# Kernel optimization log

Measured on AMD Instinct MI355X. Metric: run time of the kernel, lower is better.

## Reference

```python
import jax, jax.numpy as jnp
import numpy as np

BIG = 1e6
EPS = 1e-12


def _normalize(x):
    return x / (jnp.linalg.norm(x, axis=-1, keepdims=True) + EPS)


def _euclidean_dist(x, y):
    # x: [m, d], y: [n, d] -> [m, n]
    xx = jnp.sum(x * x, axis=1, keepdims=True)          # [m, 1]
    yy = jnp.sum(y * y, axis=1)[None, :]                # [1, n]
    d = xx + yy - 2.0 * (x @ y.T)
    return jnp.sqrt(jnp.clip(d, EPS, None))


def _cam_loss(embeddings, labels, centers_value, centers_cnt, margin):
    B, D = embeddings.shape
    C = centers_value.shape[0]

    # --- _Cup: centroid scatter-reduce update (detached in original) ---
    emb_d = jax.lax.stop_gradient(embeddings)
    sums = jax.ops.segment_sum(emb_d, labels, num_segments=C)              # [C, D]
    counts = jax.ops.segment_sum(jnp.ones((B,), emb_d.dtype), labels,
                                 num_segments=C)                           # [C]
    upd_val = jax.lax.stop_gradient(centers_value) + sums
    upd_cnt = jax.lax.stop_gradient(centers_cnt) + counts[:, None]
    centers = jnp.where(upd_cnt > 0, upd_val / jnp.maximum(upd_cnt, 1.0), 0.0)

    centers = _normalize(centers)
    emb = _normalize(embeddings)

    pd = _euclidean_dist(emb, emb)        # [B, B]
    pdc = _euclidean_dist(emb, centers)   # [B, C]

    # masks
    eye = jnp.eye(B, dtype=bool)
    labels_eq = labels[None, :] == labels[:, None]
    mask_ap = (~eye) & labels_eq          # anchor-positive [B, B]
    mask_an = ~labels_eq                  # anchor-negative [B, B]
    classes = jnp.arange(C)
    mask_ap_c = labels[:, None] == classes[None, :]   # [B, C]
    mask_an_c = ~mask_ap_c

    # hardest positive
    hp = jnp.max(mask_ap * pd, axis=1, keepdims=True)
    hp_c = jnp.max(mask_ap_c * pdc, axis=1, keepdims=True)
    hpos = jnp.maximum(hp, hp_c)                       # [B, 1]
    hpos_d = jax.lax.stop_gradient(hpos)

    # hardest negative: outside the positive boundary
    greater = pd > hpos_d
    greater_c = pdc > hpos_d
    gbm = mask_an & greater
    gbm_c = mask_an_c & greater_c
    neg_out = jnp.min(pd + BIG * (~gbm), axis=1, keepdims=True)
    neg_out_c = jnp.min(pdc + BIG * (~gbm_c), axis=1, keepdims=True)
    h_out = jnp.minimum(neg_out, neg_out_c)

    # hardest negative: inside (rows with no negative beyond the boundary)
    ms = jnp.sum(gbm, axis=1) == 0        # [B]
    ms_c = jnp.sum(gbm_c, axis=1) == 0
    neg_in = jnp.max(jnp.where(ms[:, None], pd, BIG) * mask_an,
                     axis=1, keepdims=True)
    neg_in_c = jnp.max(jnp.where(ms_c[:, None], pdc, BIG) * mask_an_c,
                       axis=1, keepdims=True)
    h_in = jnp.maximum(neg_in, neg_in_c)

    hneg = jnp.minimum(h_out, h_in)       # [B, 1]

    # MarginRankingLoss(dist_an, dist_ap, y=1, reduction='sum') / B
    loss = jnp.sum(jax.nn.relu(hpos - hneg + margin)) / B
    return loss


def setup_inputs() -> dict:
    key = jax.random.key(0)
    k1, k2 = jax.random.split(key)
    B, D, C = 4096, 2048, 1024
    return {
        "embeddings": jax.random.normal(k1, (B, D), dtype=jnp.float32),
        "labels": jax.random.randint(k2, (B,), 0, C),
        "centers_value": jnp.zeros((C, D), dtype=jnp.float32),
        "centers_cnt": jnp.zeros((C, D), dtype=jnp.float32),
        "margin": jnp.float32(1.0),
    }


def reference(embeddings, labels, centers_value, centers_cnt, margin):
    return _cam_loss(embeddings, labels, centers_value, centers_cnt, margin)
```

## Files before the change

### kernel.cpp

```cpp
#include <hip/hip_runtime.h>
#include <hip/hip_bf16.h>


typedef __attribute__((ext_vector_type(8))) short short8;
typedef __attribute__((ext_vector_type(4))) float f32x4;

#define BIGF 1e6f
#define EPSC 1e-12f

__device__ __forceinline__ float bf2f(unsigned short u){
  unsigned int x = ((unsigned int)u) << 16;
  return __uint_as_float(x);
}
__device__ __forceinline__ unsigned short f2bf(float f){
  __hip_bfloat16 h = __float2bfloat16(f);
  return *reinterpret_cast<unsigned short*>(&h);
}

#define GLL16(gptr, lptr) \
  __builtin_amdgcn_global_load_lds( \
      (const __attribute__((address_space(1))) unsigned int*)(gptr), \
      (__attribute__((address_space(3))) unsigned int*)(lptr), 16, 0, 0)

#define VMWAIT(S) asm volatile("s_waitcnt " S ::: "memory")
#define SBAR()    asm volatile("s_barrier" ::: "memory")

__global__ __launch_bounds__(256) void k_setup(const int* __restrict__ labels,
    int* cnt, int* members,
    unsigned* mn0, unsigned* mx0, unsigned* fl0,
    unsigned* mn1, unsigned* mx1, unsigned* fl1,
    int B, int C, int MMAX){
  int gid = blockIdx.x * blockDim.x + threadIdx.x;
  unsigned bigbits = __float_as_uint(BIGF);
  if (gid < B){
    mn0[gid] = bigbits; mx0[gid] = 0u; fl0[gid] = 0u;
    mn1[gid] = bigbits; mx1[gid] = 0u; fl1[gid] = 0u;
  }
  int w = threadIdx.x >> 6, lane = threadIdx.x & 63;
  int c = blockIdx.x * 4 + w;
  if (c >= C) return;
  int base = 0;
  int nit = (B + 63) >> 6;
  for (int itc = 0; itc < nit; ++itc){
    int idx = itc * 64 + lane;
    int lab = (idx < B) ? labels[idx] : -1;
    unsigned long long m = __ballot(lab == c);
    if (lab == c){
      int rk = base + (int)__popcll(m & ((1ull << lane) - 1ull));
      if (rk < MMAX) members[c * MMAX + rk] = idx;
    }
    base += (int)__popcll(m);
  }
  if (lane == 0) cnt[c] = base;
}

template<int R>
__global__ __launch_bounds__(256) void k_prep(const float* __restrict__ emb,
    const float* __restrict__ cval, const float* __restrict__ ccnt,
    const int* __restrict__ cnt, const int* __restrict__ members,
    unsigned short* __restrict__ enb, unsigned short* __restrict__ cnb,
    float* __restrict__ exx, float* __restrict__ cxx,
    int D, int MMAX, int nbNorm){
  int w = threadIdx.x >> 6, lane = threadIdx.x & 63;
  if ((int)blockIdx.x < nbNorm){
    int i = blockIdx.x * 4 + w;
    const float* row = emb + (size_t)i * D;
    float v[R][8];
    float ss = 0.f;
    #pragma unroll
    for (int r = 0; r < R; ++r){
      int base = r * 512 + lane * 8;
      float4 a = *reinterpret_cast<const float4*>(&row[base]);
      float4 b = *reinterpret_cast<const float4*>(&row[base + 4]);
      v[r][0]=a.x; v[r][1]=a.y; v[r][2]=a.z; v[r][3]=a.w;
      v[r][4]=b.x; v[r][5]=b.y; v[r][6]=b.z; v[r][7]=b.w;
      #pragma unroll
      for (int k = 0; k < 8; ++k) ss += v[r][k] * v[r][k];
    }
    #pragma unroll
    for (int s = 1; s < 64; s <<= 1) ss += __shfl_xor(ss, s);
    float inv = 1.f / (sqrtf(ss) + EPSC);
    unsigned short* orow = enb + (size_t)i * D;
    int xr = (i & 7) << 3;
    #pragma unroll
    for (int r = 0; r < R; ++r){
      int base = (r * 512 + lane * 8) ^ xr;
      short8 o;
      #pragma unroll
      for (int k = 0; k < 8; ++k) o[k] = (short)f2bf(v[r][k] * inv);
      *reinterpret_cast<short8*>(&orow[base]) = o;
    }
    if (lane == 0) exx[i] = ss * inv * inv;
  } else {
    int c = ((int)blockIdx.x - nbNorm) * 4 + w;
    int n = cnt[c], m = n < MMAX ? n : MMAX;
    float acc[R][8];
    #pragma unroll
    for (int r = 0; r < R; ++r)
      #pragma unroll
      for (int k = 0; k < 8; ++k) acc[r][k] = 0.f;
    for (int e = 0; e < m; ++e){
      const float* row = emb + (size_t)members[c * MMAX + e] * D;
      #pragma unroll
      for (int r = 0; r < R; ++r){
        int base = r * 512 + lane * 8;
        float4 a = *reinterpret_cast<const float4*>(&row[base]);
        float4 b = *reinterpret_cast<const float4*>(&row[base + 4]);
        acc[r][0]+=a.x; acc[r][1]+=a.y; acc[r][2]+=a.z; acc[r][3]+=a.w;
        acc[r][4]+=b.x; acc[r][5]+=b.y; acc[r][6]+=b.z; acc[r][7]+=b.w;
      }
    }
    float cf = (float)n;
    float ss = 0.f;
    #pragma unroll
    for (int r = 0; r < R; ++r){
      int base = r * 512 + lane * 8;
      float4 u0 = *reinterpret_cast<const float4*>(&ccnt[(size_t)c * D + base]);
      float4 u1 = *reinterpret_cast<const float4*>(&ccnt[(size_t)c * D + base + 4]);
      float4 w0 = *reinterpret_cast<const float4*>(&cval[(size_t)c * D + base]);
      float4 w1 = *reinterpret_cast<const float4*>(&cval[(size_t)c * D + base + 4]);
      float uc[8] = {u0.x,u0.y,u0.z,u0.w,u1.x,u1.y,u1.z,u1.w};
      float wv[8] = {w0.x,w0.y,w0.z,w0.w,w1.x,w1.y,w1.z,w1.w};
      #pragma unroll
      for (int k = 0; k < 8; ++k){
        float u = uc[k] + cf;
        float vv = wv[k] + acc[r][k];
        float ce = (u > 0.f) ? (vv / fmaxf(u, 1.f)) : 0.f;
        acc[r][k] = ce; ss += ce * ce;
      }
    }
    #pragma unroll
    for (int s = 1; s < 64; s <<= 1) ss += __shfl_xor(ss, s);
    float inv = 1.f / (sqrtf(ss) + EPSC);
    int xr = (c & 7) << 3;
    #pragma unroll
    for (int r = 0; r < R; ++r){
      int base = (r * 512 + lane * 8) ^ xr;
      short8 o;
      #pragma unroll
      for (int k = 0; k < 8; ++k) o[k] = (short)f2bf(acc[r][k] * inv);
      *reinterpret_cast<short8*>(&cnb[(size_t)c * D + base]) = o;
    }
    if (lane == 0) cxx[c] = ss * inv * inv;
  }
}

template<int NCH>
__global__ __launch_bounds__(256) void k_hpos(const unsigned short* __restrict__ enb,
    const unsigned short* __restrict__ cnb, const float* __restrict__ exx,
    const float* __restrict__ cxx, const int* __restrict__ labels,
    const int* __restrict__ cnt, const int* __restrict__ members,
    float* __restrict__ hpos, int D, int MMAX){
  int w = threadIdx.x >> 6, lane = threadIdx.x & 63;
  int i = blockIdx.x * 4 + w;
  int li = labels[i];
  const unsigned short* arow = enb + (size_t)i * D;
  int xri = (i & 7) << 3;
  float av[NCH][8];
  #pragma unroll
  for (int ch = 0; ch < NCH; ++ch){
    short8 a8 = *reinterpret_cast<const short8*>(&arow[(ch * 512 + lane * 8) ^ xri]);
    #pragma unroll
    for (int k = 0; k < 8; ++k) av[ch][k] = bf2f((unsigned short)a8[k]);
  }
  float xi = exx[i];
  float hp = 0.f;
  int m = cnt[li] < MMAX ? cnt[li] : MMAX;
  for (int e = 0; e < m; ++e){
    int j = members[li * MMAX + e];
    if (j == i) continue;
    const unsigned short* brow = enb + (size_t)j * D;
    int xrj = (j & 7) << 3;
    float p = 0.f;
    #pragma unroll
    for (int ch = 0; ch < NCH; ++ch){
      short8 b8 = *reinterpret_cast<const short8*>(&brow[(ch * 512 + lane * 8) ^ xrj]);
      #pragma unroll
      for (int k = 0; k < 8; ++k) p += av[ch][k] * bf2f((unsigned short)b8[k]);
    }
    #pragma unroll
    for (int s = 1; s < 64; s <<= 1) p += __shfl_xor(p, s);
    float d2 = xi + exx[j] - 2.f * p;
    hp = fmaxf(hp, sqrtf(fmaxf(d2, EPSC)));
  }
  {
    const unsigned short* brow = cnb + (size_t)li * D;
    int xrc = (li & 7) << 3;
    float p = 0.f;
    #pragma unroll
    for (int ch = 0; ch < NCH; ++ch){
      short8 b8 = *reinterpret_cast<const short8*>(&brow[(ch * 512 + lane * 8) ^ xrc]);
      #pragma unroll
      for (int k = 0; k < 8; ++k) p += av[ch][k] * bf2f((unsigned short)b8[k]);
    }
    #pragma unroll
    for (int s = 1; s < 64; s <<= 1) p += __shfl_xor(p, s);
    float d2 = xi + cxx[li] - 2.f * p;
    hp = fmaxf(hp, sqrtf(fmaxf(d2, EPSC)));
  }
  if (lane == 0) hpos[i] = hp;
}

#define PD_STAGE(SB, KIND, KT) do { \
    unsigned short* dst_ = (SB) + (KIND) * 8192 + wid * (16 * 64); \
    const unsigned short* src_ = ((KIND) < 2 \
        ? gA + (size_t)((KIND) * 128) * D \
        : gB + (size_t)(((KIND) - 2) * 128) * D) + (KT); \
    GLL16(src_, dst_); \
    GLL16(src_ + (size_t)8 * D, dst_ + 8 * 64); \
  } while (0)

#define RD_A(DST, HP) do { \
    _Pragma("unroll") \
    for (int m_ = 0; m_ < 4; ++m_){ \
      DST[m_][0] = *reinterpret_cast<const short8*>(&(HP)[aoff[m_][0]]); \
      DST[m_][1] = *reinterpret_cast<const short8*>(&(HP)[aoff[m_][1]]); \
    } } while (0)

#define RD_B(HP) do { \
    _Pragma("unroll") \
    for (int n_ = 0; n_ < 2; ++n_){ \
      b[n_][0] = *reinterpret_cast<const short8*>(&(HP)[boff[n_][0]]); \
      b[n_][1] = *reinterpret_cast<const short8*>(&(HP)[boff[n_][1]]); \
    } } while (0)

#define LGKM0() do { VMWAIT("lgkmcnt(0)"); __builtin_amdgcn_sched_barrier(0); } while (0)

#define MFMA16(AV, MH, NH) do { \
    __builtin_amdgcn_s_setprio(1); \
    _Pragma("unroll") \
    for (int m_ = 0; m_ < 4; ++m_) \
      _Pragma("unroll") \
      for (int n_ = 0; n_ < 2; ++n_) \
        _Pragma("unroll") \
        for (int ks_ = 0; ks_ < 2; ++ks_) \
          acc[MH][NH][m_][n_] = __builtin_amdgcn_mfma_f32_16x16x32_bf16( \
              AV[m_][ks_], b[n_][ks_], acc[MH][NH][m_][n_], 0, 0, 0); \
    __builtin_amdgcn_s_setprio(0); } while (0)

__global__ __launch_bounds__(512, 2) void k_pd_all(
    const unsigned short* __restrict__ enb,
    const unsigned short* __restrict__ cnb,
    const float* __restrict__ exx, const float* __restrict__ cxx,
    const int* __restrict__ labels, const float* __restrict__ hpos,
    unsigned* __restrict__ mn0, unsigned* __restrict__ mx0, unsigned* __restrict__ fl0,
    unsigned* __restrict__ mn1, unsigned* __restrict__ mx1, unsigned* __restrict__ fl1,
    int D, int nTri, int nby, int nCx)
{
  extern __shared__ unsigned short sm[];
  const int nwg = gridDim.x;
  const int orig = blockIdx.x;
  const int q8 = nwg >> 3, r8 = nwg & 7;
  const int xcd = orig & 7, idx = orig >> 3;
  const int t = (xcd < r8 ? xcd * (q8 + 1) : r8 * (q8 + 1) + (xcd - r8) * q8) + idx;

  const bool pdc = (t >= nTri);
  int bx, by;
  if (!pdc){
    if ((nby & 3) == 0){
      int gb = 0, cb = 0, rem = t;
      for (;;){
        int sz = (cb < gb) ? 16 : 10;
        if (rem < sz) break;
        rem -= sz;
        if (++cb > gb){ cb = 0; ++gb; }
      }
      if (cb < gb){
        by = gb * 4 + (rem >> 2);
        bx = cb * 4 + (rem & 3);
      } else {
        int r = 0;
        while (((r + 1) * (r + 2)) / 2 <= rem) ++r;
        by = gb * 4 + r;
        bx = cb * 4 + (rem - (r * (r + 1)) / 2);
      }
    } else {
      int b_ = (int)((sqrtf(8.f * (float)t + 1.f) - 1.f) * 0.5f);
      while ((b_ + 1) * (b_ + 2) / 2 <= t) ++b_;
      while (b_ * (b_ + 1) / 2 > t) --b_;
      by = b_; bx = t - b_ * (b_ + 1) / 2;
    }
  } else {
    int u = t - nTri;
    by = u / nCx; bx = u - by * nCx;
  }
  const unsigned short* cmat = pdc ? cnb : enb;
  const float* cxv = pdc ? cxx : exx;
  unsigned* mnv = pdc ? mn1 : mn0;
  unsigned* mxv = pdc ? mx1 : mx0;
  unsigned* flv = pdc ? fl1 : fl0;

  const int j0 = bx * 256, i0 = by * 256;
  const int tid = threadIdx.x;
  const int wid = tid >> 6, lane = tid & 63;
  const int wr = wid >> 2, wc = wid & 3;
  const int lr = lane & 15, lg = lane >> 4;

  const int srow = wid * 16 + (lane >> 3);
  const int scol = (lane & 7) * 8;
  const unsigned short* gA = enb  + (size_t)(i0 + srow) * D + scol;
  const unsigned short* gB = cmat + (size_t)(j0 + srow) * D + scol;

  int aoff[4][2], boff[2][2];
  #pragma unroll
  for (int m = 0; m < 4; ++m){
    int ra = wr * 64 + m * 16 + lr;
    #pragma unroll
    for (int ks = 0; ks < 2; ++ks)
      aoff[m][ks] = ra * 64 + ((ks * 32 + lg * 8) ^ ((ra & 7) << 3));
  }
  #pragma unroll
  for (int n = 0; n < 2; ++n){
    int rb = wc * 32 + n * 16 + lr;
    #pragma unroll
    for (int ks = 0; ks < 2; ++ks)
      boff[n][ks] = rb * 64 + ((ks * 32 + lg * 8) ^ ((rb & 7) << 3));
  }

  f32x4 acc[2][2][4][2];
  #pragma unroll
  for (int mh = 0; mh < 2; ++mh)
    #pragma unroll
    for (int nh = 0; nh < 2; ++nh)
      #pragma unroll
      for (int m = 0; m < 4; ++m)
        #pragma unroll
        for (int n = 0; n < 2; ++n)
          acc[mh][nh][m][n] = (f32x4){0.f, 0.f, 0.f, 0.f};

  short8 a0[4][2], a1[4][2], b[2][2];

  const int nt = D >> 6;
  PD_STAGE(sm, 0, 0); PD_STAGE(sm, 1, 0); PD_STAGE(sm, 2, 0); PD_STAGE(sm, 3, 0);
  VMWAIT("vmcnt(0)");
  SBAR();

  for (int it = 0; it < nt; ++it){
    const unsigned short* db = sm + (size_t)(it & 1) * 32768;
    unsigned short* sb = sm + (size_t)((it & 1) ^ 1) * 32768;
    const bool hn = (it + 1 < nt);
    const int ktn = (it + 1) << 6;
    RD_A(a0, db);
    RD_B(db + 2 * 8192);
    if (hn){ PD_STAGE(sb, 0, ktn); VMWAIT("vmcnt(4)"); } else { VMWAIT("vmcnt(4)"); }
    SBAR();
    LGKM0();
    MFMA16(a0, 0, 0);
    RD_A(a1, db + 8192);
    if (hn){ PD_STAGE(sb, 2, ktn); VMWAIT("vmcnt(4)"); } else { VMWAIT("vmcnt(2)"); }
    SBAR();
    LGKM0();
    MFMA16(a1, 1, 0);
    RD_B(db + 3 * 8192);
    if (hn){ PD_STAGE(sb, 1, ktn); VMWAIT("vmcnt(4)"); } else { VMWAIT("vmcnt(0)"); }
    SBAR();
    LGKM0();
    MFMA16(a1, 1, 1);
    if (hn){ PD_STAGE(sb, 3, ktn); VMWAIT("vmcnt(4)"); }
    SBAR();
    MFMA16(a0, 0, 1);
  }

  const bool docol = (!pdc) && (bx != by);
  int jl[2][2]; float xj[2][2], hpj[2][2];
  #pragma unroll
  for (int nh = 0; nh < 2; ++nh)
    #pragma unroll
    for (int n = 0; n < 2; ++n){
      int j = j0 + nh * 128 + wc * 32 + n * 16 + lr;
      jl[nh][n] = pdc ? j : labels[j];
      xj[nh][n] = cxv[j];
      hpj[nh][n] = docol ? hpos[j] : 0.f;
    }
  float cmn[2][2], cmx[2][2]; int cfl[2][2];
  #pragma unroll
  for (int nh = 0; nh < 2; ++nh)
    #pragma unroll
    for (int n = 0; n < 2; ++n){ cmn[nh][n] = BIGF; cmx[nh][n] = 0.f; cfl[nh][n] = 0; }

  #pragma unroll
  for (int mh = 0; mh < 2; ++mh)
    #pragma unroll
    for (int m = 0; m < 4; ++m)
      #pragma unroll
      for (int r = 0; r < 4; ++r){
        int i = i0 + mh * 128 + wr * 64 + m * 16 + lg * 4 + r;
        int li = labels[i];
        float xi = exx[i];
        float hpi = hpos[i];
        float mn = BIGF, mx = 0.f; int fl = 0;
        #pragma unroll
        for (int nh = 0; nh < 2; ++nh)
          #pragma unroll
          for (int n = 0; n < 2; ++n){
            float d2 = xi + xj[nh][n] - 2.f * acc[mh][nh][m][n][r];
            float d  = sqrtf(fmaxf(d2, EPSC));
            bool an = (li != jl[nh][n]);
            bool g  = an && (d > hpi);
            mn = fminf(mn, g ? d : BIGF);
            mx = fmaxf(mx, an ? d : 0.f);
            fl |= (g ? 1 : 0) | (an ? 2 : 0);
            if (docol){
              bool gc = an && (d > hpj[nh][n]);
              cmn[nh][n] = fminf(cmn[nh][n], gc ? d : BIGF);
              cmx[nh][n] = fmaxf(cmx[nh][n], an ? d : 0.f);
              cfl[nh][n] |= (gc ? 1 : 0) | (an ? 2 : 0);
            }
          }
        #pragma unroll
        for (int s = 1; s < 16; s <<= 1){
          mn = fminf(mn, __shfl_xor(mn, s));
          mx = fmaxf(mx, __shfl_xor(mx, s));
          fl |= __shfl_xor(fl, s);
        }
        if (lr == 0){
          atomicMin(&mnv[i], __float_as_uint(mn));
          atomicMax(&mxv[i], __float_as_uint(mx));
          if (fl) atomicOr(&flv[i], (unsigned)fl);
        }
      }
  if (docol){
    #pragma unroll
    for (int nh = 0; nh < 2; ++nh)
      #pragma unroll
      for (int n = 0; n < 2; ++n){
        float mn = cmn[nh][n], mx = cmx[nh][n]; int fl = cfl[nh][n];
        #pragma unroll
        for (int s = 16; s < 64; s <<= 1){
          mn = fminf(mn, __shfl_xor(mn, s));
          mx = fmaxf(mx, __shfl_xor(mx, s));
          fl |= __shfl_xor(fl, s);
        }
        if (lg == 0){
          int j = j0 + nh * 128 + wc * 32 + n * 16 + lr;
          atomicMin(&mn0[j], __float_as_uint(mn));
          atomicMax(&mx0[j], __float_as_uint(mx));
          if (fl) atomicOr(&fl0[j], (unsigned)fl);
        }
      }
  }
}

__global__ __launch_bounds__(1024) void k_final(const float* __restrict__ hpos,
    const unsigned* __restrict__ mn0, const unsigned* __restrict__ mx0,
    const unsigned* __restrict__ fl0, const unsigned* __restrict__ mn1,
    const unsigned* __restrict__ mx1, const unsigned* __restrict__ fl1,
    const float* __restrict__ margin, float* __restrict__ out, int B){
  __shared__ float red[16];
  float part = 0.f;
  float mar = margin[0];
  for (int i = threadIdx.x; i < B; i += blockDim.x){
    float h_out = fminf(__uint_as_float(mn0[i]), __uint_as_float(mn1[i]));
    unsigned f0 = fl0[i], f1 = fl1[i];
    float ni  = (!(f0 & 1u)) ? __uint_as_float(mx0[i]) : ((f0 & 2u) ? BIGF : 0.f);
    float nic = (!(f1 & 1u)) ? __uint_as_float(mx1[i]) : ((f1 & 2u) ? BIGF : 0.f);
    float h_in = fmaxf(ni, nic);
    float hneg = fminf(h_out, h_in);
    float t = hpos[i] - hneg + mar;
    part += fmaxf(t, 0.f);
  }
  #pragma unroll
  for (int s = 32; s; s >>= 1) part += __shfl_xor(part, s);
  if ((threadIdx.x & 63) == 0) red[threadIdx.x >> 6] = part;
  __syncthreads();
  if (threadIdx.x == 0){
    float tot = 0.f;
    int nw = blockDim.x >> 6;
    for (int k = 0; k < nw; ++k) tot += red[k];
    out[0] = tot / (float)B;
  }
}

extern "C" void kernel_launch(void* const* d_in, const int* in_sizes, int n_in,
                              void* d_out, int out_size, void* d_ws, size_t ws_size,
                              hipStream_t stream){
  const float* emb    = (const float*)d_in[0];
  const int*   labels = (const int*)d_in[1];
  const float* cval   = (const float*)d_in[2];
  const float* ccnt   = (const float*)d_in[3];
  const float* margin = (const float*)d_in[4];
  float* out = (float*)d_out;

  int B = in_sizes[1];
  int D = in_sizes[0] / B;
  int C = in_sizes[2] / D;
  const int MMAX = 64;

  char* ws = (char*)d_ws;
  size_t off = 0;
  auto alloc = [&](size_t bytes)->char*{
    char* p = ws + off;
    off = (off + bytes + 255) & ~(size_t)255;
    return p;
  };
  unsigned short* enb = (unsigned short*)alloc((size_t)B * D * 2);
  unsigned short* cnb = (unsigned short*)alloc((size_t)C * D * 2);
  float* exx  = (float*)alloc((size_t)B * 4);
  float* cxx  = (float*)alloc((size_t)C * 4);
  float* hpos = (float*)alloc((size_t)B * 4);
  unsigned* mn0 = (unsigned*)alloc((size_t)B * 4);
  unsigned* mx0 = (unsigned*)alloc((size_t)B * 4);
  unsigned* fl0 = (unsigned*)alloc((size_t)B * 4);
  unsigned* mn1 = (unsigned*)alloc((size_t)B * 4);
  unsigned* mx1 = (unsigned*)alloc((size_t)B * 4);
  unsigned* fl1 = (unsigned*)alloc((size_t)B * 4);
  int* cnt     = (int*)alloc((size_t)C * 4);
  int* members = (int*)alloc((size_t)C * MMAX * 4);
  (void)ws_size; (void)n_in; (void)out_size;

  hipFuncSetAttribute((const void*)k_pd_all,
                      hipFuncAttributeMaxDynamicSharedMemorySize, 131072);

  int nbSetup = (C + 3) / 4;
  int nbInit  = ((B > C ? B : C) + 255) / 256;
  if (nbInit > nbSetup) nbSetup = nbInit;
  k_setup<<<nbSetup, 256, 0, stream>>>(labels, cnt, members,
                                       mn0, mx0, fl0, mn1, mx1, fl1, B, C, MMAX);

  int nbNorm = B / 4, nbCent = C / 4;
  int R = D >> 9;
  if (R == 4){
    k_prep<4><<<nbNorm + nbCent, 256, 0, stream>>>(emb, cval, ccnt, cnt, members,
                                                   enb, cnb, exx, cxx, D, MMAX, nbNorm);
  } else if (R == 2){
    k_prep<2><<<nbNorm + nbCent, 256, 0, stream>>>(emb, cval, ccnt, cnt, members,
                                                   enb, cnb, exx, cxx, D, MMAX, nbNorm);
  } else {
    k_prep<1><<<nbNorm + nbCent, 256, 0, stream>>>(emb, cval, ccnt, cnt, members,
                                                   enb, cnb, exx, cxx, D, MMAX, nbNorm);
  }

  switch (R){
    case 1: k_hpos<1><<<B/4, 256, 0, stream>>>(enb, cnb, exx, cxx, labels, cnt, members, hpos, D, MMAX); break;
    case 2: k_hpos<2><<<B/4, 256, 0, stream>>>(enb, cnb, exx, cxx, labels, cnt, members, hpos, D, MMAX); break;
    default: k_hpos<4><<<B/4, 256, 0, stream>>>(enb, cnb, exx, cxx, labels, cnt, members, hpos, D, MMAX); break;
  }

  int nby = B / 256, nCx = C / 256;
  int nTri = nby * (nby + 1) / 2;
  k_pd_all<<<nTri + nby * nCx, 512, 131072, stream>>>(
      enb, cnb, exx, cxx, labels, hpos,
      mn0, mx0, fl0, mn1, mx1, fl1, D, nTri, nby, nCx);
  k_final<<<1, 1024, 0, stream>>>(hpos, mn0, mx0, fl0, mn1, mx1, fl1, margin, out, B);
}
```

Measured before the change: 145.8 us.

## Fuse class membership, centroid and hardest-positive into one per-class kernel

Replaces the setup, prep and per-row hardest-positive kernels with a normalize kernel and a per-class kernel. The per-class kernel builds the member list in shared memory, computes the centroid, then evaluates each member pair once (symmetric) plus the member-centroid distance, keeping the centroid in LDS. This removes one launch, the global members and count arrays, and the duplicated pair dot products. In exchange the per-class work is serialized within one wave, with only C/4 blocks, so parallelism may be lower.

```diff
diff --git a/kernel.cpp b/kernel.cpp
--- a/kernel.cpp
+++ b/kernel.cpp
@@ -25,180 +25,168 @@
 #define VMWAIT(S) asm volatile("s_waitcnt " S ::: "memory")
 #define SBAR()    asm volatile("s_barrier" ::: "memory")
 
-__global__ __launch_bounds__(256) void k_setup(const int* __restrict__ labels,
-    int* cnt, int* members,
-    unsigned* mn0, unsigned* mx0, unsigned* fl0,
-    unsigned* mn1, unsigned* mx1, unsigned* fl1,
-    int B, int C, int MMAX){
-  int gid = blockIdx.x * blockDim.x + threadIdx.x;
-  unsigned bigbits = __float_as_uint(BIGF);
-  if (gid < B){
-    mn0[gid] = bigbits; mx0[gid] = 0u; fl0[gid] = 0u;
-    mn1[gid] = bigbits; mx1[gid] = 0u; fl1[gid] = 0u;
-  }
+template<int R>
+__global__ __launch_bounds__(256) void k_norm(const float* __restrict__ emb,
+    unsigned short* __restrict__ enb, float* __restrict__ exx,
+    unsigned* __restrict__ mn0, unsigned* __restrict__ mx0, unsigned* __restrict__ fl0,
+    unsigned* __restrict__ mn1, unsigned* __restrict__ mx1, unsigned* __restrict__ fl1,
+    int D){
   int w = threadIdx.x >> 6, lane = threadIdx.x & 63;
-  int c = blockIdx.x * 4 + w;
+  int i = blockIdx.x * 4 + w;
+  if (lane == 0){
+    unsigned bigbits = __float_as_uint(BIGF);
+    mn0[i] = bigbits; mx0[i] = 0u; fl0[i] = 0u;
+    mn1[i] = bigbits; mx1[i] = 0u; fl1[i] = 0u;
+  }
+  const float* row = emb + (size_t)i * D;
+  float v[R][8];
+  float ss = 0.f;
+  #pragma unroll
+  for (int r = 0; r < R; ++r){
+    int base = r * 512 + lane * 8;
+    float4 a = *reinterpret_cast<const float4*>(&row[base]);
+    float4 b = *reinterpret_cast<const float4*>(&row[base + 4]);
+    v[r][0]=a.x; v[r][1]=a.y; v[r][2]=a.z; v[r][3]=a.w;
+    v[r][4]=b.x; v[r][5]=b.y; v[r][6]=b.z; v[r][7]=b.w;
+    #pragma unroll
+    for (int k = 0; k < 8; ++k) ss += v[r][k] * v[r][k];
+  }
+  #pragma unroll
+  for (int s = 1; s < 64; s <<= 1) ss += __shfl_xor(ss, s);
+  float inv = 1.f / (sqrtf(ss) + EPSC);
+  unsigned short* orow = enb + (size_t)i * D;
+  int xr = (i & 7) << 3;
+  #pragma unroll
+  for (int r = 0; r < R; ++r){
+    int base = (r * 512 + lane * 8) ^ xr;
+    short8 o;
+    #pragma unroll
+    for (int k = 0; k < 8; ++k) o[k] = (short)f2bf(v[r][k] * inv);
+    *reinterpret_cast<short8*>(&orow[base]) = o;
+  }
+  if (lane == 0) exx[i] = ss * inv * inv;
+}
+
+template<int R>
+__global__ __launch_bounds__(256) void k_cls(const float* __restrict__ emb,
+    const float* __restrict__ cval, const float* __restrict__ ccnt,
+    const int* __restrict__ labels, const unsigned short* __restrict__ enb,
+    const float* __restrict__ exx,
+    unsigned short* __restrict__ cnb, float* __restrict__ cxx,
+    float* __restrict__ hpos, int B, int D, int C){
+  __shared__ int memL[4][64];
+  __shared__ float hpL[4][64];
+  __shared__ unsigned short cenL[4][R * 512];
+  int wid = threadIdx.x >> 6, lane = threadIdx.x & 63;
+  int c = blockIdx.x * 4 + wid;
   if (c >= C) return;
-  int base = 0;
+  int n = 0;
   int nit = (B + 63) >> 6;
   for (int itc = 0; itc < nit; ++itc){
     int idx = itc * 64 + lane;
     int lab = (idx < B) ? labels[idx] : -1;
-    unsigned long long m = __ballot(lab == c);
+    unsigned long long bm = __ballot(lab == c);
     if (lab == c){
-      int rk = base + (int)__popcll(m & ((1ull << lane) - 1ull));
-      if (rk < MMAX) members[c * MMAX + rk] = idx;
-    }
-    base += (int)__popcll(m);
-  }
-  if (lane == 0) cnt[c] = base;
-}
-
-template<int R>
-__global__ __launch_bounds__(256) void k_prep(const float* __restrict__ emb,
-    const float* __restrict__ cval, const float* __restrict__ ccnt,
-    const int* __restrict__ cnt, const int* __restrict__ members,
-    unsigned short* __restrict__ enb, unsigned short* __restrict__ cnb,
-    float* __restrict__ exx, float* __restrict__ cxx,
-    int D, int MMAX, int nbNorm){
-  int w = threadIdx.x >> 6, lane = threadIdx.x & 63;
-  if ((int)blockIdx.x < nbNorm){
-    int i = blockIdx.x * 4 + w;
-    const float* row = emb + (size_t)i * D;
-    float v[R][8];
-    float ss = 0.f;
+      int rk = n + (int)__popcll(bm & ((1ull << lane) - 1ull));
+      if (rk < 64) memL[wid][rk] = idx;
+    }
+    n += (int)__popcll(bm);
+  }
+  int m = n < 64 ? n : 64;
+  hpL[wid][lane] = 0.f;
+  float acc[R][8];
+  #pragma unroll
+  for (int r = 0; r < R; ++r)
+    #pragma unroll
+    for (int k = 0; k < 8; ++k) acc[r][k] = 0.f;
+  for (int e = 0; e < m; ++e){
+    const float* row = emb + (size_t)memL[wid][e] * D;
     #pragma unroll
     for (int r = 0; r < R; ++r){
       int base = r * 512 + lane * 8;
       float4 a = *reinterpret_cast<const float4*>(&row[base]);
       float4 b = *reinterpret_cast<const float4*>(&row[base + 4]);
-      v[r][0]=a.x; v[r][1]=a.y; v[r][2]=a.z; v[r][3]=a.w;
-      v[r][4]=b.x; v[r][5]=b.y; v[r][6]=b.z; v[r][7]=b.w;
+      acc[r][0]+=a.x; acc[r][1]+=a.y; acc[r][2]+=a.z; acc[r][3]+=a.w;
+      acc[r][4]+=b.x; acc[r][5]+=b.y; acc[r][6]+=b.z; acc[r][7]+=b.w;
+    }
+  }
+  float cf = (float)n;
+  float ss = 0.f;
+  #pragma unroll
+  for (int r = 0; r < R; ++r){
+    int base = r * 512 + lane * 8;
+    float4 u0 = *reinterpret_cast<const float4*>(&ccnt[(size_t)c * D + base]);
+    float4 u1 = *reinterpret_cast<const float4*>(&ccnt[(size_t)c * D + base + 4]);
+    float4 w0 = *reinterpret_cast<const float4*>(&cval[(size_t)c * D + base]);
+    float4 w1 = *reinterpret_cast<const float4*>(&cval[(size_t)c * D + base + 4]);
+    float uc[8] = {u0.x,u0.y,u0.z,u0.w,u1.x,u1.y,u1.z,u1.w};
+    float wv[8] = {w0.x,w0.y,w0.z,w0.w,w1.x,w1.y,w1.z,w1.w};
+    #pragma unroll
+    for (int k = 0; k < 8; ++k){
+      float u = uc[k] + cf;
+      float vv = wv[k] + acc[r][k];
+      float ce = (u > 0.f) ? (vv / fmaxf(u, 1.f)) : 0.f;
+      acc[r][k] = ce; ss += ce * ce;
+    }
+  }
+  #pragma unroll
+  for (int s = 1; s < 64; s <<= 1) ss += __shfl_xor(ss, s);
+  float inv = 1.f / (sqrtf(ss) + EPSC);
+  float xc = ss * inv * inv;
+  int xr = (c & 7) << 3;
+  #pragma unroll
+  for (int r = 0; r < R; ++r){
+    int lin = r * 512 + lane * 8;
+    short8 o;
+    #pragma unroll
+    for (int k = 0; k < 8; ++k) o[k] = (short)f2bf(acc[r][k] * inv);
+    *reinterpret_cast<short8*>(&cnb[(size_t)c * D + (lin ^ xr)]) = o;
+    *reinterpret_cast<short8*>(&cenL[wid][lin]) = o;
+  }
+  if (lane == 0) cxx[c] = xc;
+  for (int e1 = 0; e1 < m; ++e1){
+    int i1 = memL[wid][e1];
+    int xr1 = (i1 & 7) << 3;
+    const unsigned short* row1 = enb + (size_t)i1 * D;
+    float av[R][8];
+    #pragma unroll
+    for (int r = 0; r < R; ++r){
+      short8 v = *reinterpret_cast<const short8*>(&row1[(r * 512 + lane * 8) ^ xr1]);
       #pragma unroll
-      for (int k = 0; k < 8; ++k) ss += v[r][k] * v[r][k];
-    }
-    #pragma unroll
-    for (int s = 1; s < 64; s <<= 1) ss += __shfl_xor(ss, s);
-    float inv = 1.f / (sqrtf(ss) + EPSC);
-    unsigned short* orow = enb + (size_t)i * D;
-    int xr = (i & 7) << 3;
-    #pragma unroll
-    for (int r = 0; r < R; ++r){
-      int base = (r * 512 + lane * 8) ^ xr;
-      short8 o;
+      for (int k = 0; k < 8; ++k) av[r][k] = bf2f((unsigned short)v[k]);
+    }
+    float x1 = exx[i1];
+    float hp = hpL[wid][e1];
+    for (int e2 = e1 + 1; e2 <= m; ++e2){
+      float p = 0.f, x2;
+      if (e2 < m){
+        int i2 = memL[wid][e2];
+        int xr2 = (i2 & 7) << 3;
+        const unsigned short* row2 = enb + (size_t)i2 * D;
+        #pragma unroll
+        for (int r = 0; r < R; ++r){
+          short8 v = *reinterpret_cast<const short8*>(&row2[(r * 512 + lane * 8) ^ xr2]);
+          #pragma unroll
+          for (int k = 0; k < 8; ++k) p += av[r][k] * bf2f((unsigned short)v[k]);
+        }
+        x2 = exx[i2];
+      } else {
+        #pragma unroll
+        for (int r = 0; r < R; ++r){
+          short8 v = *reinterpret_cast<const short8*>(&cenL[wid][r * 512 + lane * 8]);
+          #pragma unroll
+          for (int k = 0; k < 8; ++k) p += av[r][k] * bf2f((unsigned short)v[k]);
+        }
+        x2 = xc;
+      }
       #pragma unroll
-      for (int k = 0; k < 8; ++k) o[k] = (short)f2bf(v[r][k] * inv);
-      *reinterpret_cast<short8*>(&orow[base]) = o;
-    }
-    if (lane == 0) exx[i] = ss * inv * inv;
-  } else {
-    int c = ((int)blockIdx.x - nbNorm) * 4 + w;
-    int n = cnt[c], m = n < MMAX ? n : MMAX;
-    float acc[R][8];
-    #pragma unroll
-    for (int r = 0; r < R; ++r)
-      #pragma unroll
-      for (int k = 0; k < 8; ++k) acc[r][k] = 0.f;
-    for (int e = 0; e < m; ++e){
-      const float* row = emb + (size_t)members[c * MMAX + e] * D;
-      #pragma unroll
-      for (int r = 0; r < R; ++r){
-        int base = r * 512 + lane * 8;
-        float4 a = *reinterpret_cast<const float4*>(&row[base]);
-        float4 b = *reinterpret_cast<const float4*>(&row[base + 4]);
-        acc[r][0]+=a.x; acc[r][1]+=a.y; acc[r][2]+=a.z; acc[r][3]+=a.w;
-        acc[r][4]+=b.x; acc[r][5]+=b.y; acc[r][6]+=b.z; acc[r][7]+=b.w;
-      }
-    }
-    float cf = (float)n;
-    float ss = 0.f;
-    #pragma unroll
-    for (int r = 0; r < R; ++r){
-      int base = r * 512 + lane * 8;
-      float4 u0 = *reinterpret_cast<const float4*>(&ccnt[(size_t)c * D + base]);
-      float4 u1 = *reinterpret_cast<const float4*>(&ccnt[(size_t)c * D + base + 4]);
-      float4 w0 = *reinterpret_cast<const float4*>(&cval[(size_t)c * D + base]);
-      float4 w1 = *reinterpret_cast<const float4*>(&cval[(size_t)c * D + base + 4]);
-      float uc[8] = {u0.x,u0.y,u0.z,u0.w,u1.x,u1.y,u1.z,u1.w};
-      float wv[8] = {w0.x,w0.y,w0.z,w0.w,w1.x,w1.y,w1.z,w1.w};
-      #pragma unroll
-      for (int k = 0; k < 8; ++k){
-        float u = uc[k] + cf;
-        float vv = wv[k] + acc[r][k];
-        float ce = (u > 0.f) ? (vv / fmaxf(u, 1.f)) : 0.f;
-        acc[r][k] = ce; ss += ce * ce;
-      }
-    }
-    #pragma unroll
-    for (int s = 1; s < 64; s <<= 1) ss += __shfl_xor(ss, s);
-    float inv = 1.f / (sqrtf(ss) + EPSC);
-    int xr = (c & 7) << 3;
-    #pragma unroll
-    for (int r = 0; r < R; ++r){
-      int base = (r * 512 + lane * 8) ^ xr;
-      short8 o;
-      #pragma unroll
-      for (int k = 0; k < 8; ++k) o[k] = (short)f2bf(acc[r][k] * inv);
-      *reinterpret_cast<short8*>(&cnb[(size_t)c * D + base]) = o;
-    }
-    if (lane == 0) cxx[c] = ss * inv * inv;
-  }
-}
-
-template<int NCH>
-__global__ __launch_bounds__(256) void k_hpos(const unsigned short* __restrict__ enb,
-    const unsigned short* __restrict__ cnb, const float* __restrict__ exx,
-    const float* __restrict__ cxx, const int* __restrict__ labels,
-    const int* __restrict__ cnt, const int* __restrict__ members,
-    float* __restrict__ hpos, int D, int MMAX){
-  int w = threadIdx.x >> 6, lane = threadIdx.x & 63;
-  int i = blockIdx.x * 4 + w;
-  int li = labels[i];
-  const unsigned short* arow = enb + (size_t)i * D;
-  int xri = (i & 7) << 3;
-  float av[NCH][8];
-  #pragma unroll
-  for (int ch = 0; ch < NCH; ++ch){
-    short8 a8 = *reinterpret_cast<const short8*>(&arow[(ch * 512 + lane * 8) ^ xri]);
-    #pragma unroll
-    for (int k = 0; k < 8; ++k) av[ch][k] = bf2f((unsigned short)a8[k]);
-  }
-  float xi = exx[i];
-  float hp = 0.f;
-  int m = cnt[li] < MMAX ? cnt[li] : MMAX;
-  for (int e = 0; e < m; ++e){
-    int j = members[li * MMAX + e];
-    if (j == i) continue;
-    const unsigned short* brow = enb + (size_t)j * D;
-    int xrj = (j & 7) << 3;
-    float p = 0.f;
-    #pragma unroll
-    for (int ch = 0; ch < NCH; ++ch){
-      short8 b8 = *reinterpret_cast<const short8*>(&brow[(ch * 512 + lane * 8) ^ xrj]);
-      #pragma unroll
-      for (int k = 0; k < 8; ++k) p += av[ch][k] * bf2f((unsigned short)b8[k]);
-    }
-    #pragma unroll
-    for (int s = 1; s < 64; s <<= 1) p += __shfl_xor(p, s);
-    float d2 = xi + exx[j] - 2.f * p;
-    hp = fmaxf(hp, sqrtf(fmaxf(d2, EPSC)));
-  }
-  {
-    const unsigned short* brow = cnb + (size_t)li * D;
-    int xrc = (li & 7) << 3;
-    float p = 0.f;
-    #pragma unroll
-    for (int ch = 0; ch < NCH; ++ch){
-      short8 b8 = *reinterpret_cast<const short8*>(&brow[(ch * 512 + lane * 8) ^ xrc]);
-      #pragma unroll
-      for (int k = 0; k < 8; ++k) p += av[ch][k] * bf2f((unsigned short)b8[k]);
-    }
-    #pragma unroll
-    for (int s = 1; s < 64; s <<= 1) p += __shfl_xor(p, s);
-    float d2 = xi + cxx[li] - 2.f * p;
-    hp = fmaxf(hp, sqrtf(fmaxf(d2, EPSC)));
-  }
-  if (lane == 0) hpos[i] = hp;
+      for (int s = 1; s < 64; s <<= 1) p += __shfl_xor(p, s);
+      float d = sqrtf(fmaxf(x1 + x2 - 2.f * p, EPSC));
+      hp = fmaxf(hp, d);
+      if (e2 < m && lane == 0) hpL[wid][e2] = fmaxf(hpL[wid][e2], d);
+    }
+    if (lane == 0) hpos[i1] = hp;
+  }
 }
 
 #define PD_STAGE(SB, KIND, KT) do { \
@@ -484,7 +472,6 @@
   int B = in_sizes[1];
   int D = in_sizes[0] / B;
   int C = in_sizes[2] / D;
-  const int MMAX = 64;
 
   char* ws = (char*)d_ws;
   size_t off = 0;
@@ -504,36 +491,24 @@
   unsigned* mn1 = (unsigned*)alloc((size_t)B * 4);
   unsigned* mx1 = (unsigned*)alloc((size_t)B * 4);
   unsigned* fl1 = (unsigned*)alloc((size_t)B * 4);
-  int* cnt     = (int*)alloc((size_t)C * 4);
-  int* members = (int*)alloc((size_t)C * MMAX * 4);
   (void)ws_size; (void)n_in; (void)out_size;
 
   hipFuncSetAttribute((const void*)k_pd_all,
                       hipFuncAttributeMaxDynamicSharedMemorySize, 131072);
 
-  int nbSetup = (C + 3) / 4;
-  int nbInit  = ((B > C ? B : C) + 255) / 256;
-  if (nbInit > nbSetup) nbSetup = nbInit;
-  k_setup<<<nbSetup, 256, 0, stream>>>(labels, cnt, members,
-                                       mn0, mx0, fl0, mn1, mx1, fl1, B, C, MMAX);
-
-  int nbNorm = B / 4, nbCent = C / 4;
   int R = D >> 9;
   if (R == 4){
-    k_prep<4><<<nbNorm + nbCent, 256, 0, stream>>>(emb, cval, ccnt, cnt, members,
-                                                   enb, cnb, exx, cxx, D, MMAX, nbNorm);
+    k_norm<4><<<B/4, 256, 0, stream>>>(emb, enb, exx, mn0, mx0, fl0, mn1, mx1, fl1, D);
+    k_cls<4><<<(C + 3) / 4, 256, 0, stream>>>(emb, cval, ccnt, labels, enb, exx,
+                                              cnb, cxx, hpos, B, D, C);
   } else if (R == 2){
-    k_prep<2><<<nbNorm + nbCent, 256, 0, stream>>>(emb, cval, ccnt, cnt, members,
-                                                   enb, cnb, exx, cxx, D, MMAX, nbNorm);
+    k_norm<2><<<B/4, 256, 0, stream>>>(emb, enb, exx, mn0, mx0, fl0, mn1, mx1, fl1, D);
+    k_cls<2><<<(C + 3) / 4, 256, 0, stream>>>(emb, cval, ccnt, labels, enb, exx,
+                                              cnb, cxx, hpos, B, D, C);
   } else {
-    k_prep<1><<<nbNorm + nbCent, 256, 0, stream>>>(emb, cval, ccnt, cnt, members,
-                                                   enb, cnb, exx, cxx, D, MMAX, nbNorm);
-  }
-
-  switch (R){
-    case 1: k_hpos<1><<<B/4, 256, 0, stream>>>(enb, cnb, exx, cxx, labels, cnt, members, hpos, D, MMAX); break;
-    case 2: k_hpos<2><<<B/4, 256, 0, stream>>>(enb, cnb, exx, cxx, labels, cnt, members, hpos, D, MMAX); break;
-    default: k_hpos<4><<<B/4, 256, 0, stream>>>(enb, cnb, exx, cxx, labels, cnt, members, hpos, D, MMAX); break;
+    k_norm<1><<<B/4, 256, 0, stream>>>(emb, enb, exx, mn0, mx0, fl0, mn1, mx1, fl1, D);
+    k_cls<1><<<(C + 3) / 4, 256, 0, stream>>>(emb, cval, ccnt, labels, enb, exx,
+                                              cnb, cxx, hpos, B, D, C);
   }
 
   int nby = B / 256, nCx = C / 256;
```

Result: slower. 174.5 us (+19.7%).
